# Kernel optimization log

Hardware: AMD Instinct MI355X
Metric: run time of the kernel (lower is better)

## Reference

```python
import jax, jax.numpy as jnp
import numpy as np

BS, NCAMS, CIN, H, W = 4, 1, 256, 56, 200
MID = 128
DCH = 112  # (58-2)/0.5 depth bins
GX, GY, GZ = 128, 128, 16  # voxel grid


def setup_inputs() -> dict:
    key = jax.random.key(0)
    ks = jax.random.split(key, 32)
    f32 = jnp.float32

    def n(k, shape, scale=0.05):
        return jax.random.normal(k, shape, f32) * scale

    inp = {
        'img_feat': jax.random.normal(ks[0], (BS, NCAMS, CIN, H, W), f32),
        'scaled_pixel_size': jax.random.uniform(ks[1], (BS * NCAMS, 1), f32) * 2.0 + 0.5,
        # normalized sampling coords, slightly beyond [-1,1] to exercise zero padding
        'grids': jax.random.uniform(ks[2], (NCAMS, BS, GX, GY, GZ, 3), f32) * 2.2 - 1.1,
        # reduce_conv: Conv2d(CIN->MID,3x3,bias) + BN(affine, eval=per-channel scale/shift)
        'rc_w': n(ks[3], (MID, CIN, 3, 3)),
        'rc_b': n(ks[4], (MID,)),
        'rc_s': 1.0 + n(ks[5], (MID,)),
        'rc_t': n(ks[6], (MID,)),
        # Mlp(1 -> MID -> MID)
        'fc1_w': n(ks[7], (MID, 1), 0.5),
        'fc1_b': n(ks[8], (MID,)),
        'fc2_w': n(ks[9], (MID, MID)),
        'fc2_b': n(ks[10], (MID,)),
        # SELayer 1x1 convs (act on [N,MID,1,1] -> plain linears)
        'se_rw': n(ks[11], (MID, MID)),
        'se_rb': n(ks[12], (MID,)),
        'se_ew': n(ks[13], (MID, MID)),
        'se_eb': n(ks[14], (MID,)),
        # 3 BasicBlocks: conv3x3(no bias)+BN+ReLU+conv3x3(no bias)+BN, residual, ReLU
        'bb_w1': n(ks[15], (3, MID, MID, 3, 3)),
        'bb_s1': 1.0 + n(ks[16], (3, MID)),
        'bb_t1': n(ks[17], (3, MID)),
        'bb_w2': n(ks[18], (3, MID, MID, 3, 3)),
        'bb_s2': 1.0 + n(ks[19], (3, MID)),
        'bb_t2': n(ks[20], (3, MID)),
        # depth_pred 1x1 conv MID -> DCH
        'dp_w': n(ks[21], (DCH, MID)),
        'dp_b': n(ks[22], (DCH,)),
    }
    return inp


def _conv2d(x, w):
    return jax.lax.conv_general_dilated(x, w, (1, 1), 'SAME',
                                        dimension_numbers=('NCHW', 'OIHW', 'NCHW'))


def _aff(x, s, t):
    return x * s[None, :, None, None] + t[None, :, None, None]


def grid_sample_3d(feat, grid):
    """Trilinear grid_sample, zeros padding, align_corners=False.
    feat: [N,C,D,H,W]; grid: [N,X,Y,Z,3] with (x,y,z) in [-1,1] indexing (W,H,D).
    Returns [N,C,X,Y,Z]."""
    N, C, D, Hh, Ww = feat.shape
    ix = (grid[..., 0] + 1.0) * (Ww * 0.5) - 0.5
    iy = (grid[..., 1] + 1.0) * (Hh * 0.5) - 0.5
    iz = (grid[..., 2] + 1.0) * (D * 0.5) - 0.5
    x0 = jnp.floor(ix); y0 = jnp.floor(iy); z0 = jnp.floor(iz)
    fx, fy, fz = ix - x0, iy - y0, iz - z0

    def one(f, x0, y0, z0, fx, fy, fz):
        out = jnp.zeros((C,) + x0.shape, f.dtype)
        x0i = x0.astype(jnp.int32); y0i = y0.astype(jnp.int32); z0i = z0.astype(jnp.int32)
        for dz in (0, 1):
            for dy in (0, 1):
                for dx in (0, 1):
                    xi = x0i + dx; yi = y0i + dy; zi = z0i + dz
                    wgt = ((fx if dx else 1.0 - fx) * (fy if dy else 1.0 - fy)
                           * (fz if dz else 1.0 - fz))
                    valid = ((xi >= 0) & (xi < Ww) & (yi >= 0) & (yi < Hh)
                             & (zi >= 0) & (zi < D))
                    v = f[:, jnp.clip(zi, 0, D - 1), jnp.clip(yi, 0, Hh - 1),
                          jnp.clip(xi, 0, Ww - 1)]
                    out = out + v * (wgt * valid)[None]
        return out

    return jax.vmap(one)(feat, x0, y0, z0, fx, fy, fz)


def reference(img_feat, scaled_pixel_size, grids, rc_w, rc_b, rc_s, rc_t,
              fc1_w, fc1_b, fc2_w, fc2_b, se_rw, se_rb, se_ew, se_eb,
              bb_w1, bb_s1, bb_t1, bb_w2, bb_s2, bb_t2, dp_w, dp_b):
    bs, n_cams, c, h, w = img_feat.shape
    x = img_feat.reshape(bs * n_cams, c, h, w)
    # DepthNet (infer_mode): reduce_conv
    x = jax.nn.relu(_aff(_conv2d(x, rc_w) + rc_b[None, :, None, None], rc_s, rc_t))
    # Mlp on scaled_pixel_size + SE gating
    hmid = jax.nn.relu(scaled_pixel_size @ fc1_w.T + fc1_b) @ fc2_w.T + fc2_b
    se = jax.nn.relu(hmid @ se_rw.T + se_rb) @ se_ew.T + se_eb
    x = x * jax.nn.sigmoid(se)[:, :, None, None]
    # 3 BasicBlocks
    for i in range(3):
        y = jax.nn.relu(_aff(_conv2d(x, bb_w1[i]), bb_s1[i], bb_t1[i]))
        y = _aff(_conv2d(y, bb_w2[i]), bb_s2[i], bb_t2[i])
        x = jax.nn.relu(x + y)
    # depth_pred 1x1 conv, softmax over depth bins
    depth_feat = jnp.einsum('nchw,dc->ndhw', x, dp_w) + dp_b[None, :, None, None]
    depth = jax.nn.softmax(depth_feat, axis=1)
    depth = depth.reshape(bs, n_cams, 1, DCH, h, w)
    # per-camera frustum -> voxel bilinear sampling
    all_voxel_features = []
    for i in range(n_cams):
        all_voxel_features.append(grid_sample_3d(depth[:, i], grids[i]))
    agg = all_voxel_features[0]  # n_cams == 1 path in original forward
    return agg  # [bs, 1, GX, GY, GZ]
```

## Files before the change

kernel.cpp:

```cpp
#include <hip/hip_runtime.h>
#include <math.h>

typedef _Float16 v8h __attribute__((ext_vector_type(8)));
typedef float v4f __attribute__((ext_vector_type(4)));
typedef float v16f __attribute__((ext_vector_type(16)));

__global__ void __launch_bounds__(256) prep_kernel(
    const float* __restrict__ rc_w, const float* __restrict__ bb_w1,
    const float* __restrict__ bb_w2, const float* __restrict__ dp_w,
    const float* __restrict__ img, const float* __restrict__ sps,
    const float* __restrict__ fc1_w, const float* __restrict__ fc1_b,
    const float* __restrict__ fc2_w, const float* __restrict__ fc2_b,
    const float* __restrict__ se_rw, const float* __restrict__ se_rb,
    const float* __restrict__ se_ew, const float* __restrict__ se_eb,
    _Float16* __restrict__ wrc, _Float16* __restrict__ wbb,
    _Float16* __restrict__ wdp, _Float16* __restrict__ act16,
    float* __restrict__ sig) {
  const int bx = blockIdx.x;
  const int tid = threadIdx.x;
  __shared__ float buf[128];

  if (bx < 583) {
    int slot = bx * 256 + tid;
    if (slot < 36864) {
      int co = slot & 127;
      int r = slot >> 7;
      int kh = r & 1;
      r >>= 1;
      int tap = r % 9, c16 = r / 9;
      int cibase = c16 * 16 + kh * 8;
      v8h o;
#pragma unroll
      for (int j = 0; j < 8; ++j)
        o[j] = (_Float16)rc_w[((size_t)co * 256 + cibase + j) * 9 + tap];
      *(v8h*)(wrc + (size_t)slot * 8) = o;
    } else if (slot < 147456) {
      int s2 = slot - 36864;
      int blk = s2 / 18432, r2 = s2 - blk * 18432;
      int co = r2 & 127;
      int r = r2 >> 7;
      int kh = r & 1;
      r >>= 1;
      int tap = r % 9, c16 = r / 9;
      int cibase = c16 * 16 + kh * 8;
      const float* src = (blk < 3) ? (bb_w1 + (size_t)blk * 147456)
                                   : (bb_w2 + (size_t)(blk - 3) * 147456);
      int cslot = (blk < 3) ? (2 * blk) : (2 * (blk - 3) + 1);
      v8h o;
#pragma unroll
      for (int j = 0; j < 8; ++j)
        o[j] = (_Float16)src[((size_t)co * 128 + cibase + j) * 9 + tap];
      *(v8h*)(wbb + ((size_t)cslot * 18432 + r2) * 8) = o;
    } else if (slot < 149248) {
      int s3 = slot - 147456;
      v8h o;
#pragma unroll
      for (int j = 0; j < 8; ++j) o[j] = (_Float16)dp_w[(size_t)s3 * 8 + j];
      *(v8h*)(wdp + (size_t)s3 * 8) = o;
    }
  } else if (bx == 583) {
    const int j = tid;
    const bool on = j < 128;
    for (int b = 0; b < 4; ++b) {
      float h1 = 0.f;
      if (on) h1 = fmaxf(sps[b] * fc1_w[j] + fc1_b[j], 0.f);
      __syncthreads();
      if (on) buf[j] = h1;
      __syncthreads();
      float hm = 0.f;
      if (on) {
        hm = fc2_b[j];
        for (int k = 0; k < 128; ++k) hm += buf[k] * fc2_w[j * 128 + k];
      }
      __syncthreads();
      if (on) buf[j] = hm;
      __syncthreads();
      float t = 0.f;
      if (on) {
        t = se_rb[j];
        for (int k = 0; k < 128; ++k) t += buf[k] * se_rw[j * 128 + k];
        t = fmaxf(t, 0.f);
      }
      __syncthreads();
      if (on) buf[j] = t;
      __syncthreads();
      if (on) {
        float se = se_eb[j];
        for (int k = 0; k < 128; ++k) se += buf[k] * se_ew[j * 128 + k];
        sig[b * 128 + j] = 1.f / (1.f + expf(-se));
      }
      __syncthreads();
    }
  } else {
    const int bid = bx - 584;
    const int n = bid / 56, h = bid - n * 56;
    const int w = tid;
    if (w < 200) {
      const float* ip = img + ((size_t)n * 256 * 56 + h) * 200 + w;
      _Float16* op = act16 + (((size_t)n * 56 + h) * 200 + w) * 256;
#pragma unroll 4
      for (int c8 = 0; c8 < 32; ++c8) {
        v8h o;
#pragma unroll
        for (int j = 0; j < 8; ++j)
          o[j] = (_Float16)ip[(size_t)(c8 * 8 + j) * 11200];
        *(v8h*)(op + c8 * 8) = o;
      }
    }
  }
}

template <int CIN, int MODE>
__global__ void __launch_bounds__(256, 2) conv3x3_kernel(
    const _Float16* __restrict__ act, const _Float16* __restrict__ wr,
    const _Float16* __restrict__ xprev, const float* __restrict__ bias,
    const float* __restrict__ sc, const float* __restrict__ tr,
    const float* __restrict__ sig_se, _Float16* __restrict__ out) {
  constexpr int NCH = CIN / 16;
  const int wt = blockIdx.x, ht = blockIdx.y;
  const int n = blockIdx.z >> 1, cg = blockIdx.z & 1;
  const int h0 = ht * 8, w0 = wt * 32;
  const int tid = threadIdx.x;
  const int wave = tid >> 6, lane = tid & 63;
  const int l31 = lane & 31, khalf = lane >> 5;

  __shared__ alignas(16) _Float16 ldsA[2][2 * 340 * 8];
  __shared__ alignas(16) _Float16 ldsB[2][1152 * 8];

  size_t goffA[3];
  int loffA[3];
  bool exA[3], okA[3];
#pragma unroll
  for (int it = 0; it < 3; ++it) {
    int slot = it * 256 + tid;
    int pos = slot >> 1, part = slot & 1;
    int hh = pos / 34, ww = pos - hh * 34;
    int gh = h0 - 1 + hh, gw = w0 - 1 + ww;
    exA[it] = slot < 680;
    bool inimg = (unsigned)gh < 56u && (unsigned)gw < 200u;
    okA[it] = exA[it] && inimg;
    loffA[it] = (part * 340 + pos) * 8;
    int ghc = okA[it] ? gh : 0, gwc = okA[it] ? gw : 0;
    goffA[it] = (((size_t)n * 56 + ghc) * 200 + gwc) * CIN + part * 8;
  }
  size_t goffB[5];
  int loffB[5];
  bool exB[5];
#pragma unroll
  for (int it = 0; it < 5; ++it) {
    int slot = it * 256 + tid;
    exB[it] = slot < 1152;
    int s = exB[it] ? slot : 0;
    int tap = s >> 7, kh = (s >> 6) & 1, co = s & 63;
    goffB[it] = (((size_t)(tap * 2 + kh)) * 128 + cg * 64 + co) * 8;
    loffB[it] = s * 8;
  }

  const v8h zero8 = {(_Float16)0, (_Float16)0, (_Float16)0, (_Float16)0,
                     (_Float16)0, (_Float16)0, (_Float16)0, (_Float16)0};
  v8h preA[3], preB[5];
#pragma unroll
  for (int it = 0; it < 3; ++it) preA[it] = okA[it] ? *(const v8h*)(act + goffA[it]) : zero8;
#pragma unroll
  for (int it = 0; it < 5; ++it) preB[it] = *(const v8h*)(wr + goffB[it]);

  v16f acc[2][2];
#pragma unroll
  for (int mt = 0; mt < 2; ++mt)
#pragma unroll
    for (int nt = 0; nt < 2; ++nt)
#pragma unroll
      for (int r = 0; r < 16; ++r) acc[mt][nt][r] = 0.f;

#pragma unroll 1
  for (int c = 0; c < NCH; ++c) {
    _Float16* aB = &ldsA[c & 1][0];
    _Float16* bB = &ldsB[c & 1][0];
#pragma unroll
    for (int it = 0; it < 3; ++it)
      if (exA[it]) *(v8h*)(aB + loffA[it]) = preA[it];
#pragma unroll
    for (int it = 0; it < 5; ++it)
      if (exB[it]) *(v8h*)(bB + loffB[it]) = preB[it];
    __syncthreads();
    if (c + 1 < NCH) {
#pragma unroll
      for (int it = 0; it < 3; ++it)
        preA[it] = okA[it] ? *(const v8h*)(act + goffA[it] + (size_t)(c + 1) * 16) : zero8;
#pragma unroll
      for (int it = 0; it < 5; ++it)
        preB[it] = *(const v8h*)(wr + goffB[it] + (size_t)(c + 1) * 18432);
    }
#pragma unroll
    for (int dy = 0; dy < 3; ++dy) {
#pragma unroll
      for (int dx = 0; dx < 3; ++dx) {
        const int tap = dy * 3 + dx;
        v8h bfrag[2];
        bfrag[0] = *(const v8h*)(bB + (tap * 128 + khalf * 64 + l31) * 8);
        bfrag[1] = *(const v8h*)(bB + (tap * 128 + khalf * 64 + 32 + l31) * 8);
#pragma unroll
        for (int mt = 0; mt < 2; ++mt) {
          const int pos = (wave * 2 + mt + dy) * 34 + l31 + dx;
          v8h afrag = *(const v8h*)(aB + (khalf * 340 + pos) * 8);
#pragma unroll
          for (int nt = 0; nt < 2; ++nt)
            acc[mt][nt] =
                __builtin_amdgcn_mfma_f32_32x32x16_f16(afrag, bfrag[nt], acc[mt][nt], 0, 0, 0);
        }
      }
    }
  }

#pragma unroll
  for (int mt = 0; mt < 2; ++mt) {
    const int h = h0 + wave * 2 + mt;
#pragma unroll
    for (int nt = 0; nt < 2; ++nt) {
      const int cc = cg * 64 + nt * 32 + l31;
      const float s = sc[cc], t = tr[cc];
      float bb = 0.f, sg = 1.f;
      if constexpr (MODE == 0) {
        bb = bias[cc];
        sg = sig_se[n * 128 + cc];
      }
#pragma unroll
      for (int r = 0; r < 16; ++r) {
        const int m = (r & 3) + 8 * (r >> 2) + 4 * khalf;
        const int w = w0 + m;
        if (w < 200) {
          float v = acc[mt][nt][r];
          size_t oidx = (((size_t)n * 56 + h) * 200 + w) * 128 + cc;
          if constexpr (MODE == 0) v = fmaxf((v + bb) * s + t, 0.f) * sg;
          if constexpr (MODE == 1) v = fmaxf(v * s + t, 0.f);
          if constexpr (MODE == 2) v = fmaxf((float)xprev[oidx] + v * s + t, 0.f);
          out[oidx] = (_Float16)v;
        }
      }
    }
  }
}

__global__ void __launch_bounds__(256) depth_proj_softmax_kernel(
    const _Float16* __restrict__ x, const _Float16* __restrict__ wdp,
    const float* __restrict__ dp_b, _Float16* __restrict__ depth) {
  const int wave = threadIdx.x >> 6, lane = threadIdx.x & 63;
  const int q = lane >> 4, l16 = lane & 15;
  const int pos0 = blockIdx.x * 64 + wave * 16;

  v4f acc[7];
#pragma unroll
  for (int nt = 0; nt < 7; ++nt) {
    float bv = dp_b[nt * 16 + l16];
    acc[nt] = {bv, bv, bv, bv};
  }
#pragma unroll
  for (int c0 = 0; c0 < 128; c0 += 32) {
    v8h a = *(const v8h*)(x + (size_t)(pos0 + l16) * 128 + c0 + q * 8);
#pragma unroll
    for (int nt = 0; nt < 7; ++nt) {
      v8h b = *(const v8h*)(wdp + (size_t)(nt * 16 + l16) * 128 + c0 + q * 8);
      acc[nt] = __builtin_amdgcn_mfma_f32_16x16x32_f16(a, b, acc[nt], 0, 0, 0);
    }
  }
  float m[4];
#pragma unroll
  for (int r = 0; r < 4; ++r) {
    m[r] = acc[0][r];
#pragma unroll
    for (int nt = 1; nt < 7; ++nt) m[r] = fmaxf(m[r], acc[nt][r]);
  }
#pragma unroll
  for (int off = 1; off < 16; off <<= 1)
#pragma unroll
    for (int r = 0; r < 4; ++r) m[r] = fmaxf(m[r], __shfl_xor(m[r], off));
  float s[4] = {0.f, 0.f, 0.f, 0.f};
#pragma unroll
  for (int nt = 0; nt < 7; ++nt)
#pragma unroll
    for (int r = 0; r < 4; ++r) {
      float e = expf(acc[nt][r] - m[r]);
      acc[nt][r] = e;
      s[r] += e;
    }
#pragma unroll
  for (int off = 1; off < 16; off <<= 1)
#pragma unroll
    for (int r = 0; r < 4; ++r) s[r] += __shfl_xor(s[r], off);
#pragma unroll
  for (int r = 0; r < 4; ++r) {
    const float inv = 1.f / s[r];
    const size_t p = pos0 + q * 4 + r;
#pragma unroll
    for (int nt = 0; nt < 7; ++nt)
      depth[p * 112 + nt * 16 + l16] = (_Float16)(acc[nt][r] * inv);
  }
}

__global__ void __launch_bounds__(256) gridsample_kernel(
    const float* __restrict__ grids, const _Float16* __restrict__ depth,
    float* __restrict__ out) {
  const int i = blockIdx.x * 256 + threadIdx.x;
  const int n = i >> 18;
  const float gx = grids[(size_t)i * 3];
  const float gy = grids[(size_t)i * 3 + 1];
  const float gz = grids[(size_t)i * 3 + 2];
  const float ix = (gx + 1.f) * 100.f - 0.5f;
  const float iy = (gy + 1.f) * 28.f - 0.5f;
  const float iz = (gz + 1.f) * 56.f - 0.5f;
  const float xf = floorf(ix), yf = floorf(iy), zf = floorf(iz);
  const int x0 = (int)xf, y0 = (int)yf, z0 = (int)zf;
  const float fx = ix - xf, fy = iy - yf, fz = iz - zf;
  const bool zv0 = (unsigned)z0 < 112u;
  const bool zv1 = (unsigned)(z0 + 1) < 112u;
  const float wz0 = 1.f - fz, wz1 = fz;
  float acc = 0.f;
#pragma unroll
  for (int dy = 0; dy < 2; ++dy) {
    const int yi = y0 + dy;
    const float wy = dy ? fy : 1.f - fy;
#pragma unroll
    for (int dx = 0; dx < 2; ++dx) {
      const int xi = x0 + dx;
      const float wx = dx ? fx : 1.f - fx;
      if ((unsigned)xi < 200u && (unsigned)yi < 56u) {
        const _Float16* bp = depth + ((size_t)n * 11200 + yi * 200 + xi) * 112;
        float v0 = zv0 ? (float)bp[z0] : 0.f;
        float v1 = zv1 ? (float)bp[z0 + 1] : 0.f;
        acc += (wx * wy) * (wz0 * v0 + wz1 * v1);
      }
    }
  }
  out[i] = acc;
}

extern "C" void kernel_launch(void* const* d_in, const int* in_sizes, int n_in,
                              void* d_out, int out_size, void* d_ws, size_t ws_size,
                              hipStream_t stream) {
  (void)in_sizes; (void)n_in; (void)out_size; (void)ws_size;
  const float* img = (const float*)d_in[0];
  const float* sps = (const float*)d_in[1];
  const float* grids = (const float*)d_in[2];
  const float* rc_w = (const float*)d_in[3];
  const float* rc_b = (const float*)d_in[4];
  const float* rc_s = (const float*)d_in[5];
  const float* rc_t = (const float*)d_in[6];
  const float* fc1_w = (const float*)d_in[7];
  const float* fc1_b = (const float*)d_in[8];
  const float* fc2_w = (const float*)d_in[9];
  const float* fc2_b = (const float*)d_in[10];
  const float* se_rw = (const float*)d_in[11];
  const float* se_rb = (const float*)d_in[12];
  const float* se_ew = (const float*)d_in[13];
  const float* se_eb = (const float*)d_in[14];
  const float* bb_w1 = (const float*)d_in[15];
  const float* bb_s1 = (const float*)d_in[16];
  const float* bb_t1 = (const float*)d_in[17];
  const float* bb_w2 = (const float*)d_in[18];
  const float* bb_s2 = (const float*)d_in[19];
  const float* bb_t2 = (const float*)d_in[20];
  const float* dp_w = (const float*)d_in[21];
  const float* dp_b = (const float*)d_in[22];
  float* outp = (float*)d_out;

  char* ws = (char*)d_ws;
  _Float16* act16 = (_Float16*)(ws + 0);
  _Float16* depth16 = (_Float16*)(ws + 0);
  _Float16* xa = (_Float16*)(ws + 23068672);
  _Float16* xb = (_Float16*)(ws + 23068672 + 11534336);
  _Float16* yb = (_Float16*)(ws + 23068672 + 2 * 11534336);
  _Float16* wrc = (_Float16*)(ws + 57671680);
  _Float16* wdp = (_Float16*)(ws + 57671680 + 589824);
  _Float16* wbb = (_Float16*)(ws + 58327040);
  float* sig = (float*)(ws + 58327040 + 1769472);

  prep_kernel<<<dim3(808), 256, 0, stream>>>(
      rc_w, bb_w1, bb_w2, dp_w, img, sps, fc1_w, fc1_b, fc2_w, fc2_b, se_rw, se_rb,
      se_ew, se_eb, wrc, wbb, wdp, act16, sig);

  dim3 cgrid(7, 7, 8);
  conv3x3_kernel<256, 0><<<cgrid, 256, 0, stream>>>(act16, wrc, nullptr, rc_b, rc_s,
                                                    rc_t, sig, xa);
  _Float16* xcur = xa;
  _Float16* xnxt = xb;
  for (int i = 0; i < 3; ++i) {
    conv3x3_kernel<128, 1><<<cgrid, 256, 0, stream>>>(
        xcur, wbb + (size_t)(2 * i) * 147456, nullptr, nullptr, bb_s1 + i * 128,
        bb_t1 + i * 128, nullptr, yb);
    conv3x3_kernel<128, 2><<<cgrid, 256, 0, stream>>>(
        yb, wbb + (size_t)(2 * i + 1) * 147456, xcur, nullptr, bb_s2 + i * 128,
        bb_t2 + i * 128, nullptr, xnxt);
    _Float16* t = xcur;
    xcur = xnxt;
    xnxt = t;
  }

  depth_proj_softmax_kernel<<<dim3(700), 256, 0, stream>>>(xcur, wdp, dp_b, depth16);
  gridsample_kernel<<<dim3(4096), 256, 0, stream>>>(grids, depth16, outp);
}
```

Measured before the change: 425.7 us.

## Halve conv tile height to double block count, split prep transpose by channel quarters

The conv3x3 kernel now processes 4 output rows per block with 128 threads (2 waves) instead of 8 rows with 256 threads, doubling the grid to 7x14x8 blocks. The aim is better occupancy and load balance on the GPU's compute units, where 392 blocks left the machine underfilled. The trade-offs are more halo reloading per output (6 of every 4 rows loaded) and each thread now staging 9 weight vectors per channel chunk. Global offsets are narrowed to 32-bit ints with a per-image base pointer. The prep transpose is also split into four channel quarters per row, giving it more blocks and shorter loops.

```diff
diff --git a/kernel.cpp b/kernel.cpp
--- a/kernel.cpp
+++ b/kernel.cpp
@@ -93,13 +93,15 @@
     }
   } else {
     const int bid = bx - 584;
-    const int n = bid / 56, h = bid - n * 56;
+    const int n = bid / 224;
+    const int rem = bid - n * 224;
+    const int h = rem >> 2, cq = rem & 3;
     const int w = tid;
     if (w < 200) {
-      const float* ip = img + ((size_t)n * 256 * 56 + h) * 200 + w;
-      _Float16* op = act16 + (((size_t)n * 56 + h) * 200 + w) * 256;
-#pragma unroll 4
-      for (int c8 = 0; c8 < 32; ++c8) {
+      const float* ip = img + (((size_t)n * 256 + cq * 64) * 56 + h) * 200 + w;
+      _Float16* op = act16 + (((size_t)n * 56 + h) * 200 + w) * 256 + cq * 64;
+#pragma unroll 2
+      for (int c8 = 0; c8 < 8; ++c8) {
         v8h o;
 #pragma unroll
         for (int j = 0; j < 8; ++j)
@@ -111,7 +113,7 @@
 }
 
 template <int CIN, int MODE>
-__global__ void __launch_bounds__(256, 2) conv3x3_kernel(
+__global__ void __launch_bounds__(128, 2) conv3x3_kernel(
     const _Float16* __restrict__ act, const _Float16* __restrict__ wr,
     const _Float16* __restrict__ xprev, const float* __restrict__ bias,
     const float* __restrict__ sc, const float* __restrict__ tr,
@@ -119,50 +121,47 @@
   constexpr int NCH = CIN / 16;
   const int wt = blockIdx.x, ht = blockIdx.y;
   const int n = blockIdx.z >> 1, cg = blockIdx.z & 1;
-  const int h0 = ht * 8, w0 = wt * 32;
+  const int h0 = ht * 4, w0 = wt * 32;
   const int tid = threadIdx.x;
   const int wave = tid >> 6, lane = tid & 63;
   const int l31 = lane & 31, khalf = lane >> 5;
 
-  __shared__ alignas(16) _Float16 ldsA[2][2 * 340 * 8];
+  __shared__ alignas(16) _Float16 ldsA[2][2 * 204 * 8];
   __shared__ alignas(16) _Float16 ldsB[2][1152 * 8];
 
-  size_t goffA[3];
-  int loffA[3];
-  bool exA[3], okA[3];
-#pragma unroll
-  for (int it = 0; it < 3; ++it) {
-    int slot = it * 256 + tid;
+  const _Float16* actn = act + (size_t)n * 56 * 200 * CIN;
+
+  int goffA[4], loffA[4];
+  bool exA[4], okA[4];
+#pragma unroll
+  for (int it = 0; it < 4; ++it) {
+    int slot = it * 128 + tid;
     int pos = slot >> 1, part = slot & 1;
     int hh = pos / 34, ww = pos - hh * 34;
     int gh = h0 - 1 + hh, gw = w0 - 1 + ww;
-    exA[it] = slot < 680;
+    exA[it] = slot < 408;
     bool inimg = (unsigned)gh < 56u && (unsigned)gw < 200u;
     okA[it] = exA[it] && inimg;
-    loffA[it] = (part * 340 + pos) * 8;
+    loffA[it] = (part * 204 + pos) * 8;
     int ghc = okA[it] ? gh : 0, gwc = okA[it] ? gw : 0;
-    goffA[it] = (((size_t)n * 56 + ghc) * 200 + gwc) * CIN + part * 8;
-  }
-  size_t goffB[5];
-  int loffB[5];
-  bool exB[5];
-#pragma unroll
-  for (int it = 0; it < 5; ++it) {
-    int slot = it * 256 + tid;
-    exB[it] = slot < 1152;
-    int s = exB[it] ? slot : 0;
-    int tap = s >> 7, kh = (s >> 6) & 1, co = s & 63;
-    goffB[it] = (((size_t)(tap * 2 + kh)) * 128 + cg * 64 + co) * 8;
-    loffB[it] = s * 8;
+    goffA[it] = (ghc * 200 + gwc) * CIN + part * 8;
+  }
+  int goffB[9], loffB[9];
+#pragma unroll
+  for (int it = 0; it < 9; ++it) {
+    int slot = it * 128 + tid;
+    int tap = slot >> 7, kh = (slot >> 6) & 1, co = slot & 63;
+    goffB[it] = ((tap * 2 + kh) * 128 + cg * 64 + co) * 8;
+    loffB[it] = slot * 8;
   }
 
   const v8h zero8 = {(_Float16)0, (_Float16)0, (_Float16)0, (_Float16)0,
                      (_Float16)0, (_Float16)0, (_Float16)0, (_Float16)0};
-  v8h preA[3], preB[5];
-#pragma unroll
-  for (int it = 0; it < 3; ++it) preA[it] = okA[it] ? *(const v8h*)(act + goffA[it]) : zero8;
-#pragma unroll
-  for (int it = 0; it < 5; ++it) preB[it] = *(const v8h*)(wr + goffB[it]);
+  v8h preA[4], preB[9];
+#pragma unroll
+  for (int it = 0; it < 4; ++it) preA[it] = okA[it] ? *(const v8h*)(actn + goffA[it]) : zero8;
+#pragma unroll
+  for (int it = 0; it < 9; ++it) preB[it] = *(const v8h*)(wr + goffB[it]);
 
   v16f acc[2][2];
 #pragma unroll
@@ -177,19 +176,18 @@
     _Float16* aB = &ldsA[c & 1][0];
     _Float16* bB = &ldsB[c & 1][0];
 #pragma unroll
-    for (int it = 0; it < 3; ++it)
+    for (int it = 0; it < 4; ++it)
       if (exA[it]) *(v8h*)(aB + loffA[it]) = preA[it];
 #pragma unroll
-    for (int it = 0; it < 5; ++it)
-      if (exB[it]) *(v8h*)(bB + loffB[it]) = preB[it];
+    for (int it = 0; it < 9; ++it) *(v8h*)(bB + loffB[it]) = preB[it];
     __syncthreads();
     if (c + 1 < NCH) {
 #pragma unroll
-      for (int it = 0; it < 3; ++it)
-        preA[it] = okA[it] ? *(const v8h*)(act + goffA[it] + (size_t)(c + 1) * 16) : zero8;
-#pragma unroll
-      for (int it = 0; it < 5; ++it)
-        preB[it] = *(const v8h*)(wr + goffB[it] + (size_t)(c + 1) * 18432);
+      for (int it = 0; it < 4; ++it)
+        preA[it] = okA[it] ? *(const v8h*)(actn + goffA[it] + (c + 1) * 16) : zero8;
+#pragma unroll
+      for (int it = 0; it < 9; ++it)
+        preB[it] = *(const v8h*)(wr + goffB[it] + (c + 1) * 18432);
     }
 #pragma unroll
     for (int dy = 0; dy < 3; ++dy) {
@@ -202,7 +200,7 @@
 #pragma unroll
         for (int mt = 0; mt < 2; ++mt) {
           const int pos = (wave * 2 + mt + dy) * 34 + l31 + dx;
-          v8h afrag = *(const v8h*)(aB + (khalf * 340 + pos) * 8);
+          v8h afrag = *(const v8h*)(aB + (khalf * 204 + pos) * 8);
 #pragma unroll
           for (int nt = 0; nt < 2; ++nt)
             acc[mt][nt] =
@@ -374,20 +372,20 @@
   _Float16* wbb = (_Float16*)(ws + 58327040);
   float* sig = (float*)(ws + 58327040 + 1769472);
 
-  prep_kernel<<<dim3(808), 256, 0, stream>>>(
+  prep_kernel<<<dim3(1480), 256, 0, stream>>>(
       rc_w, bb_w1, bb_w2, dp_w, img, sps, fc1_w, fc1_b, fc2_w, fc2_b, se_rw, se_rb,
       se_ew, se_eb, wrc, wbb, wdp, act16, sig);
 
-  dim3 cgrid(7, 7, 8);
-  conv3x3_kernel<256, 0><<<cgrid, 256, 0, stream>>>(act16, wrc, nullptr, rc_b, rc_s,
+  dim3 cgrid(7, 14, 8);
+  conv3x3_kernel<256, 0><<<cgrid, 128, 0, stream>>>(act16, wrc, nullptr, rc_b, rc_s,
                                                     rc_t, sig, xa);
   _Float16* xcur = xa;
   _Float16* xnxt = xb;
   for (int i = 0; i < 3; ++i) {
-    conv3x3_kernel<128, 1><<<cgrid, 256, 0, stream>>>(
+    conv3x3_kernel<128, 1><<<cgrid, 128, 0, stream>>>(
         xcur, wbb + (size_t)(2 * i) * 147456, nullptr, nullptr, bb_s1 + i * 128,
         bb_t1 + i * 128, nullptr, yb);
-    conv3x3_kernel<128, 2><<<cgrid, 256, 0, stream>>>(
+    conv3x3_kernel<128, 2><<<cgrid, 128, 0, stream>>>(
         yb, wbb + (size_t)(2 * i + 1) * 147456, xcur, nullptr, bb_s2 + i * 128,
         bb_t2 + i * 128, nullptr, xnxt);
     _Float16* t = xcur;
```

Measured after the change: 520.6 us. 22.3% more time.
